# Kernel tuning notes

Hardware: AMD Instinct MI355X
Metric: run time of the kernel (lower is better)

Reference implementation:

```python
import jax, jax.numpy as jnp
import numpy as np

N, K, D, H, F = 4, 2048, 512, 8, 2048
Dh = D // H  # per-head dim_q = dim_v = dim_out = 64
EPS = 1e-10


def _uinit(k, shape, fan_sum):
    c = (6.0 / fan_sum) ** 0.5
    return jax.random.uniform(k, shape, jnp.float32, -c, c)


def setup_inputs() -> dict:
    key = jax.random.key(0)
    ks = jax.random.split(key, 8)
    x = jax.random.normal(ks[0], (N, K, D), jnp.float32)
    # per-head projection weights, stacked over heads: (H, D, Dh)
    Wq = _uinit(ks[1], (H, D, Dh), D + Dh)
    Wk = _uinit(ks[2], (H, D, Dh), D + Dh)
    Wv = _uinit(ks[3], (H, D, Dh), D + Dh)
    bq = jnp.zeros((H, Dh), jnp.float32)
    bk = jnp.zeros((H, Dh), jnp.float32)
    bv = jnp.zeros((H, Dh), jnp.float32)
    Wo = _uinit(ks[4], (H * Dh, D), H * Dh + D)
    bo = jnp.zeros((D,), jnp.float32)
    W1 = _uinit(ks[5], (D, F), D + F)
    b1 = jnp.zeros((F,), jnp.float32)
    W2 = _uinit(ks[6], (F, D), F + D)
    b2 = jnp.zeros((D,), jnp.float32)
    g1 = jnp.ones((D,), jnp.float32)
    be1 = jnp.zeros((D,), jnp.float32)
    g2 = jnp.ones((D,), jnp.float32)
    be2 = jnp.zeros((D,), jnp.float32)
    # causal mask: True = masked position (masked_fill semantics)
    mask = jnp.broadcast_to(jnp.triu(jnp.ones((K, K), bool), 1), (N, K, K))
    return dict(x=x, Wq=Wq, bq=bq, Wk=Wk, bk=bk, Wv=Wv, bv=bv, Wo=Wo, bo=bo,
                W1=W1, b1=b1, W2=W2, b2=b2, g1=g1, be1=be1, g2=g2, be2=be2,
                mask=mask)


def _layer_norm(x, g, b):
    m = x.mean(-1, keepdims=True)
    v = ((x - m) ** 2).mean(-1, keepdims=True)
    return g * (x - m) / jnp.sqrt(v + EPS) + b


def _block(x, Wq, bq, Wk, bk, Wv, bv, Wo, bo, W1, b1, W2, b2, g1, be1, g2, be2, mask):
    # per-head projections: (N, H, K, Dh)
    q = jnp.einsum('nkd,hde->nhke', x, Wq) + bq[None, :, None, :]
    k = jnp.einsum('nkd,hde->nhke', x, Wk) + bk[None, :, None, :]
    v = jnp.einsum('nkd,hde->nhke', x, Wv) + bv[None, :, None, :]
    # full score matrix (N, H, K, K) -- faithful to bmm-softmax-bmm
    s = jnp.einsum('nhqe,nhke->nhqk', q, k) / (Dh ** 0.5)
    s = jnp.where(mask[:, None], -1e9, s)
    w = jax.nn.softmax(s, axis=-1)
    att = jnp.einsum('nhqk,nhke->nhqe', w, v)
    att = att.transpose(0, 2, 1, 3).reshape(N, K, H * Dh)  # concat heads
    att = att @ Wo + bo
    h1 = _layer_norm(x + att, g1, be1)
    ff = jax.nn.relu(h1 @ W1 + b1) @ W2 + b2
    return _layer_norm(h1 + ff, g2, be2)


def reference(x, Wq, bq, Wk, bk, Wv, bv, Wo, bo, W1, b1, W2, b2, g1, be1, g2, be2, mask):
    return _block(x, Wq, bq, Wk, bk, Wv, bv, Wo, bo, W1, b1, W2, b2, g1, be1, g2, be2, mask)
```

## Files before the change

kernel.cpp:

```cpp
#include <hip/hip_runtime.h>
#include <cstdint>

typedef unsigned short u16;
typedef __bf16 bf16x8 __attribute__((ext_vector_type(8)));
typedef float f32x4 __attribute__((ext_vector_type(4)));
struct __align__(8) U2 { unsigned x, y; };

#define NEG_INF (-__builtin_inff())

__device__ __forceinline__ u16 f2bf(float f) {
  unsigned u = __builtin_bit_cast(unsigned, f);
  u += 0x7FFFu + ((u >> 16) & 1u);
  return (u16)(u >> 16);
}
__device__ __forceinline__ float bf2f(u16 b) {
  unsigned u = (unsigned)b << 16;
  return __builtin_bit_cast(float, u);
}
__device__ __forceinline__ u16 bfbits(__bf16 x) { return __builtin_bit_cast(u16, x); }
__device__ __forceinline__ unsigned pk2(float a, float b) {
  u16 lo = bfbits((__bf16)a), hi = bfbits((__bf16)b);
  return (unsigned)lo | ((unsigned)hi << 16);
}

__device__ __forceinline__ void async16(u16* dst, const u16* src) {
  __builtin_amdgcn_global_load_lds(
      (__attribute__((address_space(1))) void*)(u16*)src,
      (__attribute__((address_space(3))) void*)dst, 16, 0, 0);
}

__global__ __launch_bounds__(256) void k_cvt(const float4* __restrict__ in,
                                             uint4* __restrict__ out, int n8) {
  int i = blockIdx.x * 256 + threadIdx.x;
  if (i >= n8) return;
  float4 a = in[2 * i], b = in[2 * i + 1];
  uint4 r;
  r.x = (unsigned)f2bf(a.x) | ((unsigned)f2bf(a.y) << 16);
  r.y = (unsigned)f2bf(a.z) | ((unsigned)f2bf(a.w) << 16);
  r.z = (unsigned)f2bf(b.x) | ((unsigned)f2bf(b.y) << 16);
  r.w = (unsigned)f2bf(b.z) | ((unsigned)f2bf(b.w) << 16);
  out[i] = r;
}

__global__ __launch_bounds__(256) void k_transpose(const float* __restrict__ in,
                                                   u16* __restrict__ out, int R, int C) {
  __shared__ float t[32][65];
  int b = blockIdx.z;
  int r0 = blockIdx.y * 32, c0 = blockIdx.x * 64;
  const float* ip = in + (size_t)b * R * C;
  u16* op = out + (size_t)b * R * C;
  int tx = threadIdx.x & 63, ty = threadIdx.x >> 6;
#pragma unroll
  for (int i = 0; i < 32; i += 4) {
    int r = r0 + ty + i, c = c0 + tx;
    t[ty + i][tx] = (r < R && c < C) ? ip[(size_t)r * C + c] : 0.f;
  }
  __syncthreads();
  int cx = threadIdx.x & 31, cy = threadIdx.x >> 5;
#pragma unroll
  for (int j = 0; j < 64; j += 8) {
    int oc = c0 + cy + j, orr = r0 + cx;
    if (oc < C && orr < R) op[(size_t)oc * R + orr] = f2bf(t[cx][cy + j]);
  }
}

__global__ __launch_bounds__(256) void k_transpose_qkv(const float* __restrict__ Wq,
                                                       const float* __restrict__ Wk,
                                                       const float* __restrict__ Wv,
                                                       u16* __restrict__ out) {
  __shared__ float t[32][65];
  int z = blockIdx.z;
  const float* W = (z < 8) ? Wq : (z < 16) ? Wk : Wv;
  const float* ip = W + (size_t)(z & 7) * 32768;
  u16* op = out + (size_t)z * 32768;
  int r0 = blockIdx.y * 32;
  int tx = threadIdx.x & 63, ty = threadIdx.x >> 6;
#pragma unroll
  for (int i = 0; i < 32; i += 4)
    t[ty + i][tx] = ip[(size_t)(r0 + ty + i) * 64 + tx];
  __syncthreads();
  int cx = threadIdx.x & 31, cy = threadIdx.x >> 5;
#pragma unroll
  for (int j = 0; j < 64; j += 8)
    op[(size_t)(cy + j) * 512 + r0 + cx] = f2bf(t[cx][cy + j]);
}

__global__ __launch_bounds__(256) void k_pack_bias(const float* __restrict__ bq,
                                                   const float* __restrict__ bk,
                                                   const float* __restrict__ bv,
                                                   float* __restrict__ bpk) {
  int i = blockIdx.x * 256 + threadIdx.x;
  if (i < 1536) {
    int m = i >> 9, r = i & 511;
    const float* B = (m == 0) ? bq : (m == 1) ? bk : bv;
    bpk[i] = B[r];
  }
}

template <int EPI, int BN>
__global__ __launch_bounds__(256) void k_gemm(const u16* __restrict__ A,
                                              const u16* __restrict__ BT,
                                              const float* __restrict__ bias,
                                              u16* __restrict__ Cout,
                                              int M, int N, int Kd) {
  constexpr int HALF = 8192 + BN * 64;
  __shared__ __align__(16) u16 lds[2 * HALF];
  constexpr int NFR = BN / 32;
  constexpr int BITER = BN / 32;
  const int tid = threadIdx.x, wid = tid >> 6, lane = tid & 63;
  const int lr = lane & 15, lg = lane >> 4;
  const int wr = wid >> 1, wc = wid & 1;
  const int bid = blockIdx.x;
  const int xcd = bid & 7, local = bid >> 3;
  const int tm = (xcd * 8 + (local & 7)) * 128;
  const int tn = (local >> 3) * BN;

  f32x4 acc[4][NFR] = {};

  const int srow = lane >> 3;
  const int kb = (lane & 7) ^ srow;

  auto STAGE = [&](int buf, int kt) {
    u16* base = lds + buf * HALF;
#pragma unroll
    for (int it = 0; it < 4; ++it) {
      int rid = wid * 4 + it;
      int row = rid * 8 + srow;
      async16(base + rid * 512, A + (size_t)(tm + row) * Kd + kt + kb * 8);
    }
#pragma unroll
    for (int it = 0; it < BITER; ++it) {
      int rid = wid * BITER + it;
      int row = rid * 8 + srow;
      async16(base + 8192 + rid * 512, BT + (size_t)(tn + row) * Kd + kt + kb * 8);
    }
  };

  const int nkt = Kd >> 6;
  STAGE(0, 0);

  for (int ki = 0; ki < nkt; ++ki) {
    __builtin_amdgcn_s_barrier();
    if (ki + 1 < nkt) {
      STAGE((ki + 1) & 1, (ki + 1) << 6);
      if constexpr (BN == 128) asm volatile("s_waitcnt vmcnt(8)" ::: "memory");
      else                     asm volatile("s_waitcnt vmcnt(6)" ::: "memory");
    } else {
      asm volatile("s_waitcnt vmcnt(0)" ::: "memory");
    }
    __builtin_amdgcn_s_barrier();
    __builtin_amdgcn_sched_barrier(0);

    const char* lp = (const char*)(lds + (ki & 1) * HALF);
#pragma unroll
    for (int ks = 0; ks < 2; ++ks) {
      const int kbyte = ks * 64 + lg * 16;
      bf16x8 af[4], bfr[NFR];
#pragma unroll
      for (int mi = 0; mi < 4; ++mi) {
        int row = wr * 64 + mi * 16 + lr;
        af[mi] = *(const bf16x8*)(lp + row * 128 + (kbyte ^ ((row & 7) << 4)));
      }
#pragma unroll
      for (int nj = 0; nj < NFR; ++nj) {
        int row = wc * (BN / 2) + nj * 16 + lr;
        bfr[nj] = *(const bf16x8*)(lp + 16384 + row * 128 + (kbyte ^ ((row & 7) << 4)));
      }
#pragma unroll
      for (int mi = 0; mi < 4; ++mi)
#pragma unroll
        for (int nj = 0; nj < NFR; ++nj)
          acc[mi][nj] = __builtin_amdgcn_mfma_f32_16x16x32_bf16(af[mi], bfr[nj], acc[mi][nj], 0, 0, 0);
    }
  }

#pragma unroll
  for (int mi = 0; mi < 4; ++mi)
#pragma unroll
    for (int nj = 0; nj < NFR; ++nj) {
      int col = tn + wc * (BN / 2) + nj * 16 + lr;
      float bv = bias[col];
#pragma unroll
      for (int r = 0; r < 4; ++r) {
        int row = tm + wr * 64 + mi * 16 + lg * 4 + r;
        float v = acc[mi][nj][r] + bv;
        if (EPI == 1) v = v > 0.f ? v : 0.f;
        Cout[(size_t)row * N + col] = f2bf(v);
      }
    }
}

__global__ __launch_bounds__(256) void k_attn(const u16* __restrict__ QKV,
                                              u16* __restrict__ att) {
  __shared__ __align__(16) u16 lds[36864];
  const int lin = blockIdx.x;
  const int L = (lin & 7) * 64 + (lin >> 3);
  const int p = L & 15, nh = L >> 4;
  const int n = nh >> 3, h = nh & 7;
  const int tid = threadIdx.x, wid = tid >> 6, lane = tid & 63;
  const int lr = lane & 15, lg = lane >> 4;
  char* lp = (char*)lds;
  const u16* Qp = QKV + (size_t)(n * 2048) * 1536 + h * 64;
  const u16* Kp = Qp + 512;
  const u16* Vp = Qp + 1024;

  const int vkv = (tid & 31) * 2;
  const int vd0 = (tid >> 5) * 8;
  const int pwb = 65536 + wid * 2048;
  const float C2 = 0.18033688011112042f;
  const float B0 = 14.426950408889634f;

  for (int ph = 0; ph < 2; ++ph) {
    const int qc = (ph == 0) ? p : 31 - p;
    const int ntiles = qc + 1;
    const int qw = qc * 64 + wid * 16;
    const int qa = qw + lr;

    bf16x8 qf[2];
#pragma unroll
    for (int ks = 0; ks < 2; ++ks)
      qf[ks] = *(const bf16x8*)(Qp + (size_t)(qw + lr) * 1536 + ks * 32 + lg * 8);

    f32x4 o[4] = {};
    float lpart = 0.f;

    auto STAGE_K = [&](int t, int b) {
      const int kv0 = t * 64;
#pragma unroll
      for (int it = 0; it < 2; ++it) {
        int c = (wid * 2 + it) * 64 + lane;
        int row = c >> 3, ce = ((c & 7) ^ (row & 7)) * 8;
        async16(&lds[b * 4096 + (wid * 2 + it) * 512],
                Kp + (size_t)(kv0 + row) * 1536 + ce);
      }
    };
    auto VLAND = [&](bf16x8 va, bf16x8 vb, int b) {
#pragma unroll
      for (int jj = 0; jj < 8; ++jj) {
        int d = vd0 + jj;
        unsigned pk = (unsigned)bfbits(va[jj]) | ((unsigned)bfbits(vb[jj]) << 16);
        *(unsigned*)(lp + 32768 + b * 8192 + d * 128 + ((vkv * 2) ^ ((d & 7) << 4))) = pk;
      }
    };
    auto COMPUTE = [&](int t, int b) {
      const int kv0 = t * 64;
      f32x4 s[4] = {};
      __builtin_amdgcn_s_setprio(1);
#pragma unroll
      for (int nj = 0; nj < 4; ++nj) {
        int row = nj * 16 + lr;
#pragma unroll
        for (int ks = 0; ks < 2; ++ks) {
          bf16x8 kf = *(const bf16x8*)(lp + b * 8192 + row * 128 +
                                       ((ks * 64 + lg * 16) ^ ((row & 7) << 4)));
          s[nj] = __builtin_amdgcn_mfma_f32_16x16x32_bf16(kf, qf[ks], s[nj], 0, 0, 0);
        }
      }
      __builtin_amdgcn_s_setprio(0);

      if (t == ntiles - 1) {
#pragma unroll
        for (int nj = 0; nj < 4; ++nj) {
          int kvb = kv0 + nj * 16 + lg * 4;
#pragma unroll
          for (int r = 0; r < 4; ++r)
            if (kvb + r > qa) s[nj][r] = NEG_INF;
        }
      }

      float psum = 0.f;
#pragma unroll
      for (int nj = 0; nj < 4; ++nj)
#pragma unroll
        for (int r = 0; r < 4; ++r) {
          float pv = exp2f(fmaf(s[nj][r], C2, -B0));
          s[nj][r] = pv;
          psum += pv;
        }
      lpart += psum;

#pragma unroll
      for (int nj = 0; nj < 4; ++nj) {
        U2 val;
        val.x = pk2(s[nj][0], s[nj][1]);
        val.y = pk2(s[nj][2], s[nj][3]);
        *(U2*)(lp + pwb + lr * 128 + ((nj * 32 + lg * 8) ^ ((lr & 7) << 4))) = val;
      }

      bf16x8 pa[2];
#pragma unroll
      for (int ks = 0; ks < 2; ++ks)
        pa[ks] = *(const bf16x8*)(lp + pwb + lr * 128 +
                                  ((ks * 64 + lg * 16) ^ ((lr & 7) << 4)));
      __builtin_amdgcn_s_setprio(1);
#pragma unroll
      for (int nd = 0; nd < 4; ++nd) {
        int row = nd * 16 + lr;
#pragma unroll
        for (int ks = 0; ks < 2; ++ks) {
          bf16x8 vf = *(const bf16x8*)(lp + 32768 + b * 8192 + row * 128 +
                                       ((ks * 64 + lg * 16) ^ ((row & 7) << 4)));
          o[nd] = __builtin_amdgcn_mfma_f32_16x16x32_bf16(vf, pa[ks], o[nd], 0, 0, 0);
        }
      }
      __builtin_amdgcn_s_setprio(0);
    };

    STAGE_K(0, 0);
    if (ntiles > 1) STAGE_K(1, 1);
    {
      bf16x8 v0 = *(const bf16x8*)(Vp + (size_t)vkv * 1536 + vd0);
      bf16x8 v1 = *(const bf16x8*)(Vp + (size_t)(vkv + 1) * 1536 + vd0);
      VLAND(v0, v1, 0);
      if (ntiles > 1) {
        bf16x8 v2 = *(const bf16x8*)(Vp + (size_t)(64 + vkv) * 1536 + vd0);
        bf16x8 v3 = *(const bf16x8*)(Vp + (size_t)(64 + vkv + 1) * 1536 + vd0);
        VLAND(v2, v3, 1);
      }
    }
    __syncthreads();

    for (int t = 0; t < ntiles; t += 2) {
      const bool pre0 = (t + 2 < ntiles);
      const bool pre1 = (t + 3 < ntiles);
      bf16x8 va0, vb0, va1, vb1;
      if (pre0) {
        STAGE_K(t + 2, (t + 2) & 3);
        va0 = *(const bf16x8*)(Vp + (size_t)((t + 2) * 64 + vkv) * 1536 + vd0);
        vb0 = *(const bf16x8*)(Vp + (size_t)((t + 2) * 64 + vkv + 1) * 1536 + vd0);
      }
      if (pre1) {
        STAGE_K(t + 3, (t + 3) & 3);
        va1 = *(const bf16x8*)(Vp + (size_t)((t + 3) * 64 + vkv) * 1536 + vd0);
        vb1 = *(const bf16x8*)(Vp + (size_t)((t + 3) * 64 + vkv + 1) * 1536 + vd0);
      }

      COMPUTE(t, t & 3);
      if (t + 1 < ntiles) COMPUTE(t + 1, (t + 1) & 3);

      if (pre0) VLAND(va0, vb0, (t + 2) & 3);
      if (pre1) VLAND(va1, vb1, (t + 3) & 3);
      __syncthreads();
    }

    float lsum = lpart;
    lsum += __shfl_xor(lsum, 16);
    lsum += __shfl_xor(lsum, 32);
    float li = 1.0f / lsum;

    u16* ap = att + (size_t)(n * 2048 + qw + lr) * 512 + h * 64 + lg * 4;
#pragma unroll
    for (int nd = 0; nd < 4; ++nd) {
      U2 val;
      val.x = pk2(o[nd][0] * li, o[nd][1] * li);
      val.y = pk2(o[nd][2] * li, o[nd][3] * li);
      *(U2*)(ap + nd * 16) = val;
    }
  }
}

__global__ __launch_bounds__(256) void k_add_ln(const float* __restrict__ X,
                                                const u16* __restrict__ Yb,
                                                const float* __restrict__ gam,
                                                const float* __restrict__ bet,
                                                float* __restrict__ outf,
                                                u16* __restrict__ outb) {
  const int wid = threadIdx.x >> 6, lane = threadIdx.x & 63;
  const size_t row = (size_t)blockIdx.x * 4 + wid;
  const float4* x = (const float4*)(X + row * 512);
  float4 a0 = x[lane], a1 = x[lane + 64];
  U2 y0 = *(const U2*)(Yb + row * 512 + lane * 4);
  U2 y1 = *(const U2*)(Yb + row * 512 + 256 + lane * 4);
  float v[8];
  v[0] = a0.x + bf2f((u16)(y0.x & 0xFFFF));
  v[1] = a0.y + bf2f((u16)(y0.x >> 16));
  v[2] = a0.z + bf2f((u16)(y0.y & 0xFFFF));
  v[3] = a0.w + bf2f((u16)(y0.y >> 16));
  v[4] = a1.x + bf2f((u16)(y1.x & 0xFFFF));
  v[5] = a1.y + bf2f((u16)(y1.x >> 16));
  v[6] = a1.z + bf2f((u16)(y1.y & 0xFFFF));
  v[7] = a1.w + bf2f((u16)(y1.y >> 16));
  float s = 0.f, ss = 0.f;
#pragma unroll
  for (int i = 0; i < 8; ++i) { s += v[i]; ss += v[i] * v[i]; }
#pragma unroll
  for (int m = 1; m < 64; m <<= 1) { s += __shfl_xor(s, m); ss += __shfl_xor(ss, m); }
  float mean = s * (1.f / 512.f);
  float var = ss * (1.f / 512.f) - mean * mean;
  float rstd = rsqrtf(var + 1e-10f);
  float4 g0 = ((const float4*)gam)[lane], g1 = ((const float4*)gam)[lane + 64];
  float4 e0 = ((const float4*)bet)[lane], e1 = ((const float4*)bet)[lane + 64];
  float o[8];
  o[0] = g0.x * (v[0] - mean) * rstd + e0.x;
  o[1] = g0.y * (v[1] - mean) * rstd + e0.y;
  o[2] = g0.z * (v[2] - mean) * rstd + e0.z;
  o[3] = g0.w * (v[3] - mean) * rstd + e0.w;
  o[4] = g1.x * (v[4] - mean) * rstd + e1.x;
  o[5] = g1.y * (v[5] - mean) * rstd + e1.y;
  o[6] = g1.z * (v[6] - mean) * rstd + e1.z;
  o[7] = g1.w * (v[7] - mean) * rstd + e1.w;
  float4* of = (float4*)(outf + row * 512);
  float4 w0, w1;
  w0.x = o[0]; w0.y = o[1]; w0.z = o[2]; w0.w = o[3];
  w1.x = o[4]; w1.y = o[5]; w1.z = o[6]; w1.w = o[7];
  of[lane] = w0;
  of[lane + 64] = w1;
  if (outb) {
    u16* ob = outb + row * 512;
    U2 p0, p1;
    p0.x = pk2(o[0], o[1]); p0.y = pk2(o[2], o[3]);
    p1.x = pk2(o[4], o[5]); p1.y = pk2(o[6], o[7]);
    *(U2*)(ob + lane * 4) = p0;
    *(U2*)(ob + 256 + lane * 4) = p1;
  }
}

extern "C" void kernel_launch(void* const* d_in, const int* in_sizes, int n_in,
                              void* d_out, int out_size, void* d_ws, size_t ws_size,
                              hipStream_t stream) {
  const float* x  = (const float*)d_in[0];
  const float* Wq = (const float*)d_in[1];
  const float* bq = (const float*)d_in[2];
  const float* Wk = (const float*)d_in[3];
  const float* bk = (const float*)d_in[4];
  const float* Wv = (const float*)d_in[5];
  const float* bv = (const float*)d_in[6];
  const float* Wo = (const float*)d_in[7];
  const float* bo = (const float*)d_in[8];
  const float* W1 = (const float*)d_in[9];
  const float* b1 = (const float*)d_in[10];
  const float* W2 = (const float*)d_in[11];
  const float* b2 = (const float*)d_in[12];
  const float* g1 = (const float*)d_in[13];
  const float* be1 = (const float*)d_in[14];
  const float* g2 = (const float*)d_in[15];
  const float* be2 = (const float*)d_in[16];

  char* ws = (char*)d_ws;
  u16* xb   = (u16*)(ws + 0);
  u16* attb = (u16*)(ws + 0);
  u16* h1b  = (u16*)(ws + 0);
  u16* WqkvT = (u16*)(ws + (size_t)(8u << 20));
  u16* WoT = WqkvT + 786432;
  u16* W1T = WoT + 262144;
  u16* W2T = W1T + 1048576;
  float* bqkv = (float*)(W2T + 1048576);
  u16* QKV = (u16*)(ws + (size_t)(16u << 20));
  u16* attproj = (u16*)(ws + (size_t)(16u << 20));
  u16* ff1 = (u16*)(ws + (size_t)(16u << 20));
  u16* ffn2 = (u16*)(ws + (size_t)(50u << 20));
  float* h1f = (float*)d_out;

  k_cvt<<<2048, 256, 0, stream>>>((const float4*)x, (uint4*)xb, 524288);
  k_transpose_qkv<<<dim3(1, 16, 24), 256, 0, stream>>>(Wq, Wk, Wv, WqkvT);
  k_transpose<<<dim3(8, 16, 1), 256, 0, stream>>>(Wo, WoT, 512, 512);
  k_transpose<<<dim3(32, 16, 1), 256, 0, stream>>>(W1, W1T, 512, 2048);
  k_transpose<<<dim3(8, 64, 1), 256, 0, stream>>>(W2, W2T, 2048, 512);
  k_pack_bias<<<6, 256, 0, stream>>>(bq, bk, bv, bqkv);

  k_gemm<0, 128><<<768, 256, 0, stream>>>(xb, WqkvT, bqkv, QKV, 8192, 1536, 512);
  k_attn<<<512, 256, 0, stream>>>(QKV, attb);
  k_gemm<0, 64><<<512, 256, 0, stream>>>(attb, WoT, bo, attproj, 8192, 512, 512);
  k_add_ln<<<2048, 256, 0, stream>>>(x, attproj, g1, be1, h1f, h1b);
  k_gemm<1, 128><<<1024, 256, 0, stream>>>(h1b, W1T, b1, ff1, 8192, 2048, 512);
  k_gemm<0, 64><<<512, 256, 0, stream>>>(ff1, W2T, b2, ffn2, 8192, 512, 2048);
  k_add_ln<<<2048, 256, 0, stream>>>(h1f, ffn2, g2, be2, (float*)d_out, nullptr);
}
```

Baseline: 169.2 us.

## Merge weight prep kernels, single-buffer FFN1 GEMM, drop fp32 h1 round-trip

Combines the Wo/W1/W2/QKV transposes and bias packing into one k_prep launch to cut launch overhead. Adds a single-buffered mode to the GEMM and uses it for the FFN1 GEMM, halving its LDS footprint, presumably to raise occupancy at the cost of losing load/compute overlap. The first LayerNorm no longer writes an fp32 h1; the second LayerNorm reads the bf16 h1 as its residual, saving memory traffic but lowering residual precision.

```diff
diff --git a/kernel.cpp b/kernel.cpp
--- a/kernel.cpp
+++ b/kernel.cpp
@@ -42,69 +42,62 @@
   out[i] = r;
 }
 
-__global__ __launch_bounds__(256) void k_transpose(const float* __restrict__ in,
-                                                   u16* __restrict__ out, int R, int C) {
-  __shared__ float t[32][65];
-  int b = blockIdx.z;
-  int r0 = blockIdx.y * 32, c0 = blockIdx.x * 64;
-  const float* ip = in + (size_t)b * R * C;
-  u16* op = out + (size_t)b * R * C;
-  int tx = threadIdx.x & 63, ty = threadIdx.x >> 6;
-#pragma unroll
-  for (int i = 0; i < 32; i += 4) {
-    int r = r0 + ty + i, c = c0 + tx;
-    t[ty + i][tx] = (r < R && c < C) ? ip[(size_t)r * C + c] : 0.f;
-  }
-  __syncthreads();
-  int cx = threadIdx.x & 31, cy = threadIdx.x >> 5;
-#pragma unroll
-  for (int j = 0; j < 64; j += 8) {
-    int oc = c0 + cy + j, orr = r0 + cx;
-    if (oc < C && orr < R) op[(size_t)oc * R + orr] = f2bf(t[cx][cy + j]);
-  }
-}
-
-__global__ __launch_bounds__(256) void k_transpose_qkv(const float* __restrict__ Wq,
-                                                       const float* __restrict__ Wk,
-                                                       const float* __restrict__ Wv,
-                                                       u16* __restrict__ out) {
-  __shared__ float t[32][65];
-  int z = blockIdx.z;
-  const float* W = (z < 8) ? Wq : (z < 16) ? Wk : Wv;
-  const float* ip = W + (size_t)(z & 7) * 32768;
-  u16* op = out + (size_t)z * 32768;
-  int r0 = blockIdx.y * 32;
-  int tx = threadIdx.x & 63, ty = threadIdx.x >> 6;
-#pragma unroll
-  for (int i = 0; i < 32; i += 4)
-    t[ty + i][tx] = ip[(size_t)(r0 + ty + i) * 64 + tx];
-  __syncthreads();
-  int cx = threadIdx.x & 31, cy = threadIdx.x >> 5;
-#pragma unroll
-  for (int j = 0; j < 64; j += 8)
-    op[(size_t)(cy + j) * 512 + r0 + cx] = f2bf(t[cx][cy + j]);
-}
-
-__global__ __launch_bounds__(256) void k_pack_bias(const float* __restrict__ bq,
-                                                   const float* __restrict__ bk,
-                                                   const float* __restrict__ bv,
-                                                   float* __restrict__ bpk) {
-  int i = blockIdx.x * 256 + threadIdx.x;
-  if (i < 1536) {
+__global__ __launch_bounds__(256) void k_prep(const float* __restrict__ Wo,
+                                              const float* __restrict__ W1,
+                                              const float* __restrict__ W2,
+                                              const float* __restrict__ Wq,
+                                              const float* __restrict__ Wk,
+                                              const float* __restrict__ Wv,
+                                              const float* __restrict__ bq,
+                                              const float* __restrict__ bk,
+                                              const float* __restrict__ bv,
+                                              u16* __restrict__ WoT,
+                                              u16* __restrict__ W1T,
+                                              u16* __restrict__ W2T,
+                                              u16* __restrict__ WqkvT,
+                                              float* __restrict__ bqkv) {
+  const int b = blockIdx.x, tid = threadIdx.x;
+  if (b >= 1536) {
+    int i = (b - 1536) * 256 + tid;
     int m = i >> 9, r = i & 511;
     const float* B = (m == 0) ? bq : (m == 1) ? bk : bv;
-    bpk[i] = B[r];
-  }
-}
-
-template <int EPI, int BN>
+    bqkv[i] = B[r];
+    return;
+  }
+  __shared__ float t[32][65];
+  const float* ip;
+  u16* op;
+  int R, C, r0, c0;
+  if (b < 128)      { ip = Wo; op = WoT; R = 512;  C = 512;  c0 = (b & 7) * 64;          r0 = (b >> 3) * 32; }
+  else if (b < 640) { int i = b - 128; ip = W1; op = W1T; R = 512;  C = 2048; c0 = (i & 31) * 64; r0 = (i >> 5) * 32; }
+  else if (b < 1152){ int i = b - 640; ip = W2; op = W2T; R = 2048; C = 512;  c0 = (i & 7) * 64;  r0 = (i >> 3) * 32; }
+  else {
+    int i = b - 1152;
+    int z = i >> 4;
+    const float* W = (z < 8) ? Wq : (z < 16) ? Wk : Wv;
+    ip = W + (size_t)(z & 7) * 32768;
+    op = WqkvT + (size_t)z * 32768;
+    R = 512; C = 64; c0 = 0; r0 = (i & 15) * 32;
+  }
+  int tx = tid & 63, ty = tid >> 6;
+#pragma unroll
+  for (int i = 0; i < 32; i += 4)
+    t[ty + i][tx] = ip[(size_t)(r0 + ty + i) * C + c0 + tx];
+  __syncthreads();
+  int cx = tid & 31, cy = tid >> 5;
+#pragma unroll
+  for (int j = 0; j < 64; j += 8)
+    op[(size_t)(c0 + cy + j) * R + r0 + cx] = f2bf(t[cx][cy + j]);
+}
+
+template <bool DBUF, int EPI, int BN>
 __global__ __launch_bounds__(256) void k_gemm(const u16* __restrict__ A,
                                               const u16* __restrict__ BT,
                                               const float* __restrict__ bias,
                                               u16* __restrict__ Cout,
                                               int M, int N, int Kd) {
   constexpr int HALF = 8192 + BN * 64;
-  __shared__ __align__(16) u16 lds[2 * HALF];
+  __shared__ __align__(16) u16 lds[DBUF ? 2 * HALF : HALF];
   constexpr int NFR = BN / 32;
   constexpr int BITER = BN / 32;
   const int tid = threadIdx.x, wid = tid >> 6, lane = tid & 63;
@@ -136,22 +129,7 @@
     }
   };
 
-  const int nkt = Kd >> 6;
-  STAGE(0, 0);
-
-  for (int ki = 0; ki < nkt; ++ki) {
-    __builtin_amdgcn_s_barrier();
-    if (ki + 1 < nkt) {
-      STAGE((ki + 1) & 1, (ki + 1) << 6);
-      if constexpr (BN == 128) asm volatile("s_waitcnt vmcnt(8)" ::: "memory");
-      else                     asm volatile("s_waitcnt vmcnt(6)" ::: "memory");
-    } else {
-      asm volatile("s_waitcnt vmcnt(0)" ::: "memory");
-    }
-    __builtin_amdgcn_s_barrier();
-    __builtin_amdgcn_sched_barrier(0);
-
-    const char* lp = (const char*)(lds + (ki & 1) * HALF);
+  auto COMPUTE = [&](const char* lp) {
 #pragma unroll
     for (int ks = 0; ks < 2; ++ks) {
       const int kbyte = ks * 64 + lg * 16;
@@ -171,6 +149,31 @@
 #pragma unroll
         for (int nj = 0; nj < NFR; ++nj)
           acc[mi][nj] = __builtin_amdgcn_mfma_f32_16x16x32_bf16(af[mi], bfr[nj], acc[mi][nj], 0, 0, 0);
+    }
+  };
+
+  const int nkt = Kd >> 6;
+  if constexpr (DBUF) {
+    STAGE(0, 0);
+    for (int ki = 0; ki < nkt; ++ki) {
+      __builtin_amdgcn_s_barrier();
+      if (ki + 1 < nkt) {
+        STAGE((ki + 1) & 1, (ki + 1) << 6);
+        if constexpr (BN == 128) asm volatile("s_waitcnt vmcnt(8)" ::: "memory");
+        else                     asm volatile("s_waitcnt vmcnt(6)" ::: "memory");
+      } else {
+        asm volatile("s_waitcnt vmcnt(0)" ::: "memory");
+      }
+      __builtin_amdgcn_s_barrier();
+      __builtin_amdgcn_sched_barrier(0);
+      COMPUTE((const char*)(lds + (ki & 1) * HALF));
+    }
+  } else {
+    for (int ki = 0; ki < nkt; ++ki) {
+      STAGE(0, ki << 6);
+      __syncthreads();
+      COMPUTE((const char*)lds);
+      __syncthreads();
     }
   }
 
@@ -359,7 +362,8 @@
   }
 }
 
-__global__ __launch_bounds__(256) void k_add_ln(const float* __restrict__ X,
+template <bool XF32>
+__global__ __launch_bounds__(256) void k_add_ln(const void* __restrict__ Xp,
                                                 const u16* __restrict__ Yb,
                                                 const float* __restrict__ gam,
                                                 const float* __restrict__ bet,
@@ -367,19 +371,32 @@
                                                 u16* __restrict__ outb) {
   const int wid = threadIdx.x >> 6, lane = threadIdx.x & 63;
   const size_t row = (size_t)blockIdx.x * 4 + wid;
-  const float4* x = (const float4*)(X + row * 512);
-  float4 a0 = x[lane], a1 = x[lane + 64];
+  float xv[8];
+  if constexpr (XF32) {
+    const float4* x = (const float4*)((const float*)Xp + row * 512);
+    float4 a0 = x[lane], a1 = x[lane + 64];
+    xv[0] = a0.x; xv[1] = a0.y; xv[2] = a0.z; xv[3] = a0.w;
+    xv[4] = a1.x; xv[5] = a1.y; xv[6] = a1.z; xv[7] = a1.w;
+  } else {
+    const u16* x = (const u16*)Xp + row * 512;
+    U2 x0 = *(const U2*)(x + lane * 4);
+    U2 x1 = *(const U2*)(x + 256 + lane * 4);
+    xv[0] = bf2f((u16)(x0.x & 0xFFFF)); xv[1] = bf2f((u16)(x0.x >> 16));
+    xv[2] = bf2f((u16)(x0.y & 0xFFFF)); xv[3] = bf2f((u16)(x0.y >> 16));
+    xv[4] = bf2f((u16)(x1.x & 0xFFFF)); xv[5] = bf2f((u16)(x1.x >> 16));
+    xv[6] = bf2f((u16)(x1.y & 0xFFFF)); xv[7] = bf2f((u16)(x1.y >> 16));
+  }
   U2 y0 = *(const U2*)(Yb + row * 512 + lane * 4);
   U2 y1 = *(const U2*)(Yb + row * 512 + 256 + lane * 4);
   float v[8];
-  v[0] = a0.x + bf2f((u16)(y0.x & 0xFFFF));
-  v[1] = a0.y + bf2f((u16)(y0.x >> 16));
-  v[2] = a0.z + bf2f((u16)(y0.y & 0xFFFF));
-  v[3] = a0.w + bf2f((u16)(y0.y >> 16));
-  v[4] = a1.x + bf2f((u16)(y1.x & 0xFFFF));
-  v[5] = a1.y + bf2f((u16)(y1.x >> 16));
-  v[6] = a1.z + bf2f((u16)(y1.y & 0xFFFF));
-  v[7] = a1.w + bf2f((u16)(y1.y >> 16));
+  v[0] = xv[0] + bf2f((u16)(y0.x & 0xFFFF));
+  v[1] = xv[1] + bf2f((u16)(y0.x >> 16));
+  v[2] = xv[2] + bf2f((u16)(y0.y & 0xFFFF));
+  v[3] = xv[3] + bf2f((u16)(y0.y >> 16));
+  v[4] = xv[4] + bf2f((u16)(y1.x & 0xFFFF));
+  v[5] = xv[5] + bf2f((u16)(y1.x >> 16));
+  v[6] = xv[6] + bf2f((u16)(y1.y & 0xFFFF));
+  v[7] = xv[7] + bf2f((u16)(y1.y >> 16));
   float s = 0.f, ss = 0.f;
 #pragma unroll
   for (int i = 0; i < 8; ++i) { s += v[i]; ss += v[i] * v[i]; }
@@ -399,12 +416,14 @@
   o[5] = g1.y * (v[5] - mean) * rstd + e1.y;
   o[6] = g1.z * (v[6] - mean) * rstd + e1.z;
   o[7] = g1.w * (v[7] - mean) * rstd + e1.w;
-  float4* of = (float4*)(outf + row * 512);
-  float4 w0, w1;
-  w0.x = o[0]; w0.y = o[1]; w0.z = o[2]; w0.w = o[3];
-  w1.x = o[4]; w1.y = o[5]; w1.z = o[6]; w1.w = o[7];
-  of[lane] = w0;
-  of[lane + 64] = w1;
+  if (outf) {
+    float4* of = (float4*)(outf + row * 512);
+    float4 w0, w1;
+    w0.x = o[0]; w0.y = o[1]; w0.z = o[2]; w0.w = o[3];
+    w1.x = o[4]; w1.y = o[5]; w1.z = o[6]; w1.w = o[7];
+    of[lane] = w0;
+    of[lane + 64] = w1;
+  }
   if (outb) {
     u16* ob = outb + row * 512;
     U2 p0, p1;
@@ -449,20 +468,16 @@
   u16* attproj = (u16*)(ws + (size_t)(16u << 20));
   u16* ff1 = (u16*)(ws + (size_t)(16u << 20));
   u16* ffn2 = (u16*)(ws + (size_t)(50u << 20));
-  float* h1f = (float*)d_out;
 
   k_cvt<<<2048, 256, 0, stream>>>((const float4*)x, (uint4*)xb, 524288);
-  k_transpose_qkv<<<dim3(1, 16, 24), 256, 0, stream>>>(Wq, Wk, Wv, WqkvT);
-  k_transpose<<<dim3(8, 16, 1), 256, 0, stream>>>(Wo, WoT, 512, 512);
-  k_transpose<<<dim3(32, 16, 1), 256, 0, stream>>>(W1, W1T, 512, 2048);
-  k_transpose<<<dim3(8, 64, 1), 256, 0, stream>>>(W2, W2T, 2048, 512);
-  k_pack_bias<<<6, 256, 0, stream>>>(bq, bk, bv, bqkv);
-
-  k_gemm<0, 128><<<768, 256, 0, stream>>>(xb, WqkvT, bqkv, QKV, 8192, 1536, 512);
+  k_prep<<<1542, 256, 0, stream>>>(Wo, W1, W2, Wq, Wk, Wv, bq, bk, bv,
+                                   WoT, W1T, W2T, WqkvT, bqkv);
+
+  k_gemm<true, 0, 128><<<768, 256, 0, stream>>>(xb, WqkvT, bqkv, QKV, 8192, 1536, 512);
   k_attn<<<512, 256, 0, stream>>>(QKV, attb);
-  k_gemm<0, 64><<<512, 256, 0, stream>>>(attb, WoT, bo, attproj, 8192, 512, 512);
-  k_add_ln<<<2048, 256, 0, stream>>>(x, attproj, g1, be1, h1f, h1b);
-  k_gemm<1, 128><<<1024, 256, 0, stream>>>(h1b, W1T, b1, ff1, 8192, 2048, 512);
-  k_gemm<0, 64><<<512, 256, 0, stream>>>(ff1, W2T, b2, ffn2, 8192, 512, 2048);
-  k_add_ln<<<2048, 256, 0, stream>>>(h1f, ffn2, g2, be2, (float*)d_out, nullptr);
-}
+  k_gemm<true, 0, 64><<<512, 256, 0, stream>>>(attb, WoT, bo, attproj, 8192, 512, 512);
+  k_add_ln<true><<<2048, 256, 0, stream>>>(x, attproj, g1, be1, nullptr, h1b);
+  k_gemm<false, 1, 128><<<1024, 256, 0, stream>>>(h1b, W1T, b1, ff1, 8192, 2048, 512);
+  k_gemm<true, 0, 64><<<512, 256, 0, stream>>>(ff1, W2T, b2, ffn2, 8192, 512, 2048);
+  k_add_ln<false><<<2048, 256, 0, stream>>>(h1b, ffn2, g2, be2, (float*)d_out, nullptr);
+}
```

Result: faster. 158.5 us (-6.3%).
